# Optimization experiments

Hardware: AMD Instinct MI355X
Metric: run time of the kernel (lower is better)

## Reference

```python
import jax, jax.numpy as jnp
import numpy as np

B, N, D, H = 2, 4096, 512, 8
DH = D // H
FF = 4 * D
SCALE = D ** (-0.5)  # standard_scale=False -> dim**-0.5
EPS = 1e-5


def layernorm(x, w, b):
    mu = jnp.mean(x, axis=-1, keepdims=True)
    var = jnp.mean(jnp.square(x - mu), axis=-1, keepdims=True)
    return (x - mu) * jax.lax.rsqrt(var + EPS) * w + b


def setup_inputs() -> dict:
    key = jax.random.key(0)
    ks = jax.random.split(key, 12)
    s = lambda fin: 1.0 / np.sqrt(fin)
    return {
        "x": jax.random.normal(ks[0], (B, N, D), jnp.float32),
        "gamma": jax.random.uniform(ks[1], (B,), jnp.float32),
        "dist": jax.random.uniform(ks[2], (N, N), jnp.float32),
        "ln1_w": jnp.ones((D,), jnp.float32),
        "ln1_b": jnp.zeros((D,), jnp.float32),
        "qkv_w": jax.random.normal(ks[3], (D, 3 * D), jnp.float32) * s(D),
        "qkv_b": jnp.zeros((3 * D,), jnp.float32),
        "proj_w": jax.random.normal(ks[4], (D, D), jnp.float32) * s(D),
        "proj_b": jnp.zeros((D,), jnp.float32),
        "ln2_w": jnp.ones((D,), jnp.float32),
        "ln2_b": jnp.zeros((D,), jnp.float32),
        "fc1_w": jax.random.normal(ks[5], (D, FF), jnp.float32) * s(D),
        "fc1_b": jnp.zeros((FF,), jnp.float32),
        "fc2_w": jax.random.normal(ks[6], (FF, D), jnp.float32) * s(FF),
        "fc2_b": jnp.zeros((D,), jnp.float32),
    }


def reference(x, gamma, dist, ln1_w, ln1_b, qkv_w, qkv_b, proj_w, proj_b,
              ln2_w, ln2_b, fc1_w, fc1_b, fc2_w, fc2_b):
    # --- attention branch ---
    h = layernorm(x, ln1_w, ln1_b)                       # [B,N,D]
    qkv = h @ qkv_w + qkv_b                              # [B,N,3D]
    qkv = qkv.reshape(B, N, 3, H, DH).transpose(2, 0, 3, 1, 4)  # [3,B,H,N,DH]
    q, k, v = qkv[0], qkv[1], qkv[2]
    scores = jnp.einsum('bhnd,bhmd->bhnm', q, k) * SCALE
    scores = scores - gamma[:, None, None, None] * dist[None, None]
    w = jax.nn.softmax(scores, axis=-1)                  # [B,H,N,N]
    out = jnp.einsum('bhnm,bhmd->bhnd', w, v)            # [B,H,N,DH]
    out = out.transpose(0, 2, 1, 3).reshape(B, N, D)
    x = x + out @ proj_w + proj_b
    # --- MLP branch ---
    h = layernorm(x, ln2_w, ln2_b)
    h = jax.nn.gelu(h @ fc1_w + fc1_b, approximate=False)
    x = x + h @ fc2_w + fc2_b
    return x
```

## Files before the change

### kernel.cpp

```cpp
#include <hip/hip_runtime.h>
#include <math.h>

typedef __bf16 bf16x8 __attribute__((ext_vector_type(8)));
typedef __bf16 bf16x4 __attribute__((ext_vector_type(4)));
typedef float  f32x4  __attribute__((ext_vector_type(4)));
typedef unsigned int u32x4 __attribute__((ext_vector_type(4)));

#define B_   2
#define N_   4096
#define D_   512
#define H_   8
#define FF_  2048
#define BN_  (B_*N_)
static constexpr float SCALE_ = 0.04419417382415922f;
static constexpr float LOG2E_ = 1.44269504088896341f;
static constexpr float SCALE_L2E_ = SCALE_ * LOG2E_;

#define GLOAD_LDS16(g, l) __builtin_amdgcn_global_load_lds( \
    (const __attribute__((address_space(1))) void*)(g),     \
    (__attribute__((address_space(3))) void*)(l), 16, 0, 0)

__global__ void transpose_to_bf16(const float* __restrict__ in, __bf16* __restrict__ out,
                                  int R, int C) {
    __shared__ float tile[32][33];
    const int c0 = blockIdx.x * 32, r0 = blockIdx.y * 32;
    const int tx = threadIdx.x, ty = threadIdx.y;
#pragma unroll
    for (int i = 0; i < 4; ++i)
        tile[ty + 8*i][tx] = in[(size_t)(r0 + ty + 8*i) * C + c0 + tx];
    __syncthreads();
#pragma unroll
    for (int i = 0; i < 4; ++i)
        out[(size_t)(c0 + ty + 8*i) * R + r0 + tx] = (__bf16)tile[tx][ty + 8*i];
}

__global__ void cvt_bf16(const float* __restrict__ in, __bf16* __restrict__ out, int n4) {
    int i = blockIdx.x * blockDim.x + threadIdx.x;
    const int stride = gridDim.x * blockDim.x;
    for (; i < n4; i += stride) {
        float4 v = ((const float4*)in)[i];
        bf16x4 o;
        o[0] = (__bf16)(v.x * LOG2E_); o[1] = (__bf16)(v.y * LOG2E_);
        o[2] = (__bf16)(v.z * LOG2E_); o[3] = (__bf16)(v.w * LOG2E_);
        ((bf16x4*)out)[i] = o;
    }
}

__global__ __launch_bounds__(128)
void ln_kernel(const float* __restrict__ x, const float* __restrict__ w,
               const float* __restrict__ b, __bf16* __restrict__ out) {
    const int row = blockIdx.x, t = threadIdx.x;
    const float4 v = *(const float4*)&x[(size_t)row * 512 + t * 4];
    float s  = v.x + v.y + v.z + v.w;
    float sq = v.x*v.x + v.y*v.y + v.z*v.z + v.w*v.w;
#pragma unroll
    for (int mk = 1; mk < 64; mk <<= 1) { s += __shfl_xor(s, mk); sq += __shfl_xor(sq, mk); }
    __shared__ float ps[2][2];
    if ((t & 63) == 0) { ps[t >> 6][0] = s; ps[t >> 6][1] = sq; }
    __syncthreads();
    s = ps[0][0] + ps[1][0]; sq = ps[0][1] + ps[1][1];
    const float mu  = s * (1.0f / 512.0f);
    const float var = sq * (1.0f / 512.0f) - mu * mu;
    const float rs  = rsqrtf(var + 1e-5f);
    const float4 wv = *(const float4*)&w[t * 4];
    const float4 bv = *(const float4*)&b[t * 4];
    bf16x4 o;
    o[0] = (__bf16)((v.x - mu) * rs * wv.x + bv.x);
    o[1] = (__bf16)((v.y - mu) * rs * wv.y + bv.y);
    o[2] = (__bf16)((v.z - mu) * rs * wv.z + bv.z);
    o[3] = (__bf16)((v.w - mu) * rs * wv.w + bv.w);
    *(bf16x4*)&out[(size_t)row * 512 + t * 4] = o;
}

template<int EPI, int BNT, bool DBUF>
__global__ __launch_bounds__(256)
void gemm_bt(const __bf16* __restrict__ A, const __bf16* __restrict__ Bt,
             const float* __restrict__ bias, const float* __restrict__ resid,
             __bf16* __restrict__ outb, float* __restrict__ outf,
             int M, int N, int K) {
    constexpr int NI = BNT / 32;
    constexpr int NB = DBUF ? 2 : 1;
    __shared__ __align__(16) __bf16 As[NB][128 * 64];
    __shared__ __align__(16) __bf16 Bs[NB][BNT * 64];
    const int tid = threadIdx.x;
    const int w = tid >> 6, l = tid & 63;
    const int g = l >> 4, c = l & 15;
    const int m0 = blockIdx.y * 128, n0 = blockIdx.x * BNT;
    const int wm = (w >> 1) * 64, wn = (w & 1) * (BNT / 2);
    f32x4 acc[4][NI] = {};

    auto stage = [&](int kt, int buf) {
#pragma unroll
        for (int i = 0; i < 4; ++i) {
            const int cb = (i * 4 + w) * 64;
            const int chunk = cb + l;
            const int row = chunk >> 3, c8 = chunk & 7;
            GLOAD_LDS16(A + (size_t)(m0 + row) * K + kt + c8 * 8, As[buf] + cb * 8);
        }
#pragma unroll
        for (int i = 0; i < BNT / 32; ++i) {
            const int cb = (i * 4 + w) * 64;
            const int chunk = cb + l;
            const int row = chunk >> 3, c8 = chunk & 7;
            GLOAD_LDS16(Bt + (size_t)(n0 + row) * K + kt + c8 * 8, Bs[buf] + cb * 8);
        }
    };
    auto compute = [&](int buf) {
#pragma unroll
        for (int kk = 0; kk < 2; ++kk) {
            bf16x8 av[4], bv[NI];
#pragma unroll
            for (int mi = 0; mi < 4; ++mi)
                av[mi] = *(const bf16x8*)&As[buf][(wm + mi * 16 + c) * 64 + kk * 32 + g * 8];
#pragma unroll
            for (int ni = 0; ni < NI; ++ni)
                bv[ni] = *(const bf16x8*)&Bs[buf][(wn + ni * 16 + c) * 64 + kk * 32 + g * 8];
#pragma unroll
            for (int mi = 0; mi < 4; ++mi)
#pragma unroll
                for (int ni = 0; ni < NI; ++ni)
                    acc[mi][ni] = __builtin_amdgcn_mfma_f32_16x16x32_bf16(
                        av[mi], bv[ni], acc[mi][ni], 0, 0, 0);
        }
    };

    if constexpr (DBUF) {
        stage(0, 0);
        const int T = K / 64;
        for (int t = 0; t < T; ++t) {
            const int cur = t & 1;
            __syncthreads();
            if (t + 1 < T) stage((t + 1) * 64, cur ^ 1);
            compute(cur);
        }
    } else {
        for (int kt = 0; kt < K; kt += 64) {
            __syncthreads();
            stage(kt, 0);
            __syncthreads();
            compute(0);
        }
    }
#pragma unroll
    for (int mi = 0; mi < 4; ++mi)
#pragma unroll
        for (int ni = 0; ni < NI; ++ni)
#pragma unroll
            for (int r = 0; r < 4; ++r) {
                const int row = m0 + wm + mi * 16 + g * 4 + r;
                const int col = n0 + wn + ni * 16 + c;
                float v = acc[mi][ni][r] + bias[col];
                const size_t oidx = (size_t)row * N + col;
                if constexpr (EPI == 0) {
                    outb[oidx] = (__bf16)v;
                } else if constexpr (EPI == 1) {
                    outb[oidx] = (__bf16)(0.5f * v * (1.0f + erff(v * 0.70710678118654752f)));
                } else {
                    outf[oidx] = v + resid[oidx];
                }
            }
}

__global__ __launch_bounds__(512, 4)
void attn_kernel(const __bf16* __restrict__ qkv, const __bf16* __restrict__ distb,
                 const float* __restrict__ gamma, __bf16* __restrict__ outp) {
    __shared__ __align__(16) __bf16 Ks [64 * 64];
    __shared__ __align__(16) __bf16 Vts[64][72];
    __shared__ __align__(16) __bf16 DPs[2][128 * 64];
    const int tid = threadIdx.x;
    const int w = tid >> 6, l = tid & 63;
    const int g = l >> 4, c = l & 15;
    const int wq = w & 3, hn = w >> 2;
    const int qt = blockIdx.x, h = blockIdx.y;
    const int b = blockIdx.z;
    const float gb = gamma[b];
    const size_t tok0 = (size_t)b * N_;
    const int qrow = 16 * wq + c;
    const int wub = tid & 448;
    const int srow = tid >> 3;
    const int sd0  = (tid & 7) * 8;
    const int cswz = ((tid & 7) ^ (srow & 7)) * 8;
    const int swz  = (c & 7) << 3;

    bf16x8 qf[2][2];
#pragma unroll
    for (int t = 0; t < 2; ++t) {
        const size_t qbase = (tok0 + qt * 128 + 64 * t + qrow) * 1536 + h * 64;
#pragma unroll
        for (int kk = 0; kk < 2; ++kk) {
            const bf16x8 qv = *(const bf16x8*)&qkv[qbase + kk * 32 + g * 8];
#pragma unroll
            for (int j = 0; j < 8; ++j) qf[t][kk][j] = (__bf16)((float)qv[j] * SCALE_L2E_);
        }
    }
    bf16x8 ones;
#pragma unroll
    for (int j = 0; j < 8; ++j) ones[j] = (__bf16)1.0f;

    f32x4 acc[2][4] = {};
    f32x4 accl[2] = {};
    bf16x8 vreg;

    const size_t kvstep = (size_t)64 * 1536;
    const __bf16* gk = qkv + 512  + (tok0 + srow) * 1536 + h * 64 + cswz;
    const __bf16* gv = qkv + 1024 + (tok0 + srow) * 1536 + h * 64 + sd0;
    const __bf16* gd = distb + (size_t)(qt * 128 + srow) * N_ + cswz;

    auto issue_k = [&]() {
        GLOAD_LDS16(gk, Ks + wub * 8);
        gk += kvstep;
    };
    auto issue_d = [&](int buf) {
        GLOAD_LDS16(gd,                    DPs[buf] + wub * 8);
        GLOAD_LDS16(gd + (size_t)64 * N_,  DPs[buf] + (512 + wub) * 8);
        gd += 64;
    };
    auto issue_v = [&]() {
        vreg = *(const bf16x8*)gv;
        gv += kvstep;
    };
    auto write_vts = [&]() {
        const int kp = srow ^ sd0;
#pragma unroll
        for (int j = 0; j < 8; ++j) Vts[sd0 + j][kp] = vreg[j];
    };

    const int ktend = N_ / 64;
    issue_k();
    issue_v();
    issue_d(0);

    for (int kt = 0; kt < ktend; ++kt) {
        const int cur = kt & 1;
        __syncthreads();
        write_vts();
        if (kt + 1 < ktend) {
            issue_v();
            issue_d(cur ^ 1);
        }
        __builtin_amdgcn_sched_barrier(0);

        uint32_t W[2][2][2];
#pragma unroll
        for (int nii = 0; nii < 2; ++nii) {
            const int ni = 2 * hn + nii;
            f32x4 s0, s1;
            {
                const bf16x4 dd0 = *(const bf16x4*)
                    &DPs[cur][(qrow << 6) + ((16 * ni + 4 * g) ^ swz)];
                const bf16x4 dd1 = *(const bf16x4*)
                    &DPs[cur][((64 + qrow) << 6) + ((16 * ni + 4 * g) ^ swz)];
#pragma unroll
                for (int r = 0; r < 4; ++r) {
                    s0[r] = -gb * (float)dd0[r];
                    s1[r] = -gb * (float)dd1[r];
                }
            }
            __builtin_amdgcn_s_setprio(1);
#pragma unroll
            for (int kk = 0; kk < 2; ++kk) {
                const bf16x8 kf = *(const bf16x8*)
                    &Ks[((16 * ni + c) << 6) + ((kk * 32 + g * 8) ^ swz)];
                s0 = __builtin_amdgcn_mfma_f32_16x16x32_bf16(kf, qf[0][kk], s0, 0, 0, 0);
                s1 = __builtin_amdgcn_mfma_f32_16x16x32_bf16(kf, qf[1][kk], s1, 0, 0, 0);
            }
            __builtin_amdgcn_s_setprio(0);
#pragma unroll
            for (int t = 0; t < 2; ++t) {
                const f32x4 sv = (t == 0) ? s0 : s1;
                float pv0, pv1, pv2, pv3;
                pv0 = __builtin_amdgcn_exp2f(sv[0]);
                pv1 = __builtin_amdgcn_exp2f(sv[1]);
                pv2 = __builtin_amdgcn_exp2f(sv[2]);
                pv3 = __builtin_amdgcn_exp2f(sv[3]);
                asm("v_cvt_pk_bf16_f32 %0, %1, %2" : "=v"(W[t][nii][0]) : "v"(pv0), "v"(pv1));
                asm("v_cvt_pk_bf16_f32 %0, %1, %2" : "=v"(W[t][nii][1]) : "v"(pv2), "v"(pv3));
            }
        }
        bf16x8 pa[2];
#pragma unroll
        for (int t = 0; t < 2; ++t) {
#pragma unroll
            for (int p = 0; p < 2; ++p) {
                asm("v_permlane32_swap_b32 %0, %1"
                    : "+v"(W[t][0][p]), "+v"(W[t][1][p]));
                asm("v_permlane16_swap_b32 %0, %1"
                    : "+v"(W[t][0][p]), "+v"(W[t][1][p]));
            }
            const u32x4 words = {W[t][0][0], W[t][0][1], W[t][1][0], W[t][1][1]};
            pa[t] = __builtin_bit_cast(bf16x8, words);
        }
        __builtin_amdgcn_sched_barrier(0);
        asm volatile("s_waitcnt lgkmcnt(0)\n\ts_barrier" ::: "memory");
        __builtin_amdgcn_sched_barrier(0);
        if (kt + 1 < ktend) issue_k();

        __builtin_amdgcn_s_setprio(1);
        accl[0] = __builtin_amdgcn_mfma_f32_16x16x32_bf16(ones, pa[0], accl[0], 0, 0, 0);
        accl[1] = __builtin_amdgcn_mfma_f32_16x16x32_bf16(ones, pa[1], accl[1], 0, 0, 0);
#pragma unroll
        for (int di = 0; di < 4; ++di) {
            const int d = 16 * di + c;
            const int kp = (hn * 32 + g * 8) ^ ((d >> 3) << 3);
            const bf16x8 vb = *(const bf16x8*)&Vts[d][kp];
            acc[0][di] = __builtin_amdgcn_mfma_f32_16x16x32_bf16(vb, pa[0], acc[0][di], 0, 0, 0);
            acc[1][di] = __builtin_amdgcn_mfma_f32_16x16x32_bf16(vb, pa[1], acc[1][di], 0, 0, 0);
        }
        __builtin_amdgcn_s_setprio(0);
    }

    __syncthreads();
    float* sacc = (float*)&DPs[0][0];
    float* sl   = (float*)&Ks[0];
    const int slot = wq * 64 + l;
    if (hn == 0) {
#pragma unroll
        for (int t = 0; t < 2; ++t) {
            sl[slot * 2 + t] = accl[t][0];
#pragma unroll
            for (int di = 0; di < 4; ++di)
                *(f32x4*)&sacc[(slot * 8 + t * 4 + di) * 4] = acc[t][di];
        }
    }
    __syncthreads();
    if (hn == 1) {
#pragma unroll
        for (int t = 0; t < 2; ++t) {
            const float rl = 1.0f / (accl[t][0] + sl[slot * 2 + t]);
            const int q = qt * 128 + 64 * t + qrow;
#pragma unroll
            for (int di = 0; di < 4; ++di) {
                const f32x4 oa = acc[t][di] + *(const f32x4*)&sacc[(slot * 8 + t * 4 + di) * 4];
                bf16x4 o;
#pragma unroll
                for (int r = 0; r < 4; ++r) o[r] = (__bf16)(oa[r] * rl);
                *(bf16x4*)&outp[((size_t)(b * N_ + q)) * 512 + h * 64 + 16 * di + 4 * g] = o;
            }
        }
    }
}

extern "C" void kernel_launch(void* const* d_in, const int* in_sizes, int n_in,
                              void* d_out, int out_size, void* d_ws, size_t ws_size,
                              hipStream_t stream) {
    (void)in_sizes; (void)n_in; (void)out_size; (void)ws_size;
    const float* x      = (const float*)d_in[0];
    const float* gamma  = (const float*)d_in[1];
    const float* dist   = (const float*)d_in[2];
    const float* ln1_w  = (const float*)d_in[3];
    const float* ln1_b  = (const float*)d_in[4];
    const float* qkv_w  = (const float*)d_in[5];
    const float* qkv_b  = (const float*)d_in[6];
    const float* proj_w = (const float*)d_in[7];
    const float* proj_b = (const float*)d_in[8];
    const float* ln2_w  = (const float*)d_in[9];
    const float* ln2_b  = (const float*)d_in[10];
    const float* fc1_w  = (const float*)d_in[11];
    const float* fc1_b  = (const float*)d_in[12];
    const float* fc2_w  = (const float*)d_in[13];
    const float* fc2_b  = (const float*)d_in[14];
    float* out = (float*)d_out;

    char* ws = (char*)d_ws;
    size_t off = 0;
    auto alloc = [&](size_t bytes) {
        void* p = ws + off; off = (off + bytes + 255) & ~(size_t)255; return p;
    };
    __bf16* distbf  = (__bf16*)alloc((size_t)N_ * N_ * 2);
    __bf16* qkv_wt  = (__bf16*)alloc((size_t)1536 * 512 * 2);
    __bf16* proj_wt = (__bf16*)alloc((size_t)512 * 512 * 2);
    __bf16* fc1_wt  = (__bf16*)alloc((size_t)2048 * 512 * 2);
    __bf16* fc2_wt  = (__bf16*)alloc((size_t)512 * 2048 * 2);
    __bf16* hbuf    = (__bf16*)alloc((size_t)BN_ * 512 * 2);
    __bf16* qkvbuf  = (__bf16*)alloc((size_t)BN_ * 1536 * 2);
    __bf16* attnbuf = (__bf16*)alloc((size_t)BN_ * 512 * 2);
    float*  x1buf   = (float*) alloc((size_t)BN_ * 512 * 4);
    __bf16* h2buf   = (__bf16*)alloc((size_t)BN_ * 512 * 2);
    __bf16* ffbuf   = (__bf16*)alloc((size_t)BN_ * 2048 * 2);

    const dim3 tb(32, 8);
    transpose_to_bf16<<<dim3(1536/32,  512/32), tb, 0, stream>>>(qkv_w,  qkv_wt,  512, 1536);
    transpose_to_bf16<<<dim3( 512/32,  512/32), tb, 0, stream>>>(proj_w, proj_wt, 512,  512);
    transpose_to_bf16<<<dim3(2048/32,  512/32), tb, 0, stream>>>(fc1_w,  fc1_wt,  512, 2048);
    transpose_to_bf16<<<dim3( 512/32, 2048/32), tb, 0, stream>>>(fc2_w,  fc2_wt, 2048,  512);
    cvt_bf16<<<2048, 256, 0, stream>>>(dist, distbf, N_ * N_ / 4);

    ln_kernel<<<BN_, 128, 0, stream>>>(x, ln1_w, ln1_b, hbuf);
    gemm_bt<0,128,false><<<dim3(1536/128, BN_/128), 256, 0, stream>>>(
        hbuf, qkv_wt, qkv_b, nullptr, qkvbuf, nullptr, BN_, 1536, 512);
    attn_kernel<<<dim3(32, 8, 2), 512, 0, stream>>>(qkvbuf, distbf, gamma, attnbuf);
    gemm_bt<2,64,true><<<dim3(512/64, BN_/128), 256, 0, stream>>>(
        attnbuf, proj_wt, proj_b, x, nullptr, x1buf, BN_, 512, 512);
    ln_kernel<<<BN_, 128, 0, stream>>>(x1buf, ln2_w, ln2_b, h2buf);
    gemm_bt<1,128,false><<<dim3(2048/128, BN_/128), 256, 0, stream>>>(
        h2buf, fc1_wt, fc1_b, nullptr, ffbuf, nullptr, BN_, 2048, 512);
    gemm_bt<2,64,true><<<dim3(512/64, BN_/128), 256, 0, stream>>>(
        ffbuf, fc2_wt, fc2_b, x1buf, nullptr, out, BN_, 512, 2048);
}
```

Baseline: 284.5 us.

## Stage GEMM epilogue through LDS for vectorized stores; drop double buffering

Reworks the GEMM epilogue so each wave first writes its accumulator tile into LDS, reusing the A tile buffer. It then reads the tile back in row-contiguous chunks and issues 16-byte vector stores and residual loads, replacing scattered scalar per-element stores. It also adds a min-blocks-per-CU hint of 4 to launch_bounds and switches the two N=512 GEMMs from double-buffered to single-buffered staging to cut LDS use and raise occupancy. The trade-off is an extra LDS round trip plus a barrier in the epilogue, and loss of load/compute overlap in the proj and fc2 GEMMs.

```diff
diff --git a/kernel.cpp b/kernel.cpp
--- a/kernel.cpp
+++ b/kernel.cpp
@@ -73,7 +73,7 @@
 }
 
 template<int EPI, int BNT, bool DBUF>
-__global__ __launch_bounds__(256)
+__global__ __launch_bounds__(256, 4)
 void gemm_bt(const __bf16* __restrict__ A, const __bf16* __restrict__ Bt,
              const float* __restrict__ bias, const float* __restrict__ resid,
              __bf16* __restrict__ outb, float* __restrict__ outf,
@@ -141,24 +141,53 @@
             compute(0);
         }
     }
-#pragma unroll
-    for (int mi = 0; mi < 4; ++mi)
-#pragma unroll
-        for (int ni = 0; ni < NI; ++ni)
-#pragma unroll
-            for (int r = 0; r < 4; ++r) {
-                const int row = m0 + wm + mi * 16 + g * 4 + r;
-                const int col = n0 + wn + ni * 16 + c;
-                float v = acc[mi][ni][r] + bias[col];
-                const size_t oidx = (size_t)row * N + col;
-                if constexpr (EPI == 0) {
-                    outb[oidx] = (__bf16)v;
-                } else if constexpr (EPI == 1) {
-                    outb[oidx] = (__bf16)(0.5f * v * (1.0f + erff(v * 0.70710678118654752f)));
-                } else {
-                    outf[oidx] = v + resid[oidx];
+
+    __syncthreads();
+    if constexpr (EPI == 2) {
+        constexpr int LDW = NI * 16 + 4;
+        float* ep = (float*)&As[0][0] + w * (16 * LDW);
+#pragma unroll
+        for (int mi = 0; mi < 4; ++mi) {
+#pragma unroll
+            for (int ni = 0; ni < NI; ++ni)
+#pragma unroll
+                for (int r = 0; r < 4; ++r)
+                    ep[(g * 4 + r) * LDW + ni * 16 + c] =
+                        acc[mi][ni][r] + bias[n0 + wn + ni * 16 + c];
+#pragma unroll
+            for (int rnd = 0; rnd < NI; ++rnd) {
+                const int idx = rnd * 64 + l;
+                const int rr = idx >> 3, cc = idx & 7;
+                const f32x4 vv = *(const f32x4*)&ep[rr * LDW + cc * 4];
+                const size_t oidx = (size_t)(m0 + wm + mi * 16 + rr) * N + n0 + wn + cc * 4;
+                const f32x4 rv = *(const f32x4*)&resid[oidx];
+                *(f32x4*)&outf[oidx] = vv + rv;
+            }
+        }
+    } else {
+        constexpr int LDW = NI * 16 + 8;
+        __bf16* ep = &As[0][0] + w * (16 * LDW);
+#pragma unroll
+        for (int mi = 0; mi < 4; ++mi) {
+#pragma unroll
+            for (int ni = 0; ni < NI; ++ni)
+#pragma unroll
+                for (int r = 0; r < 4; ++r) {
+                    float v = acc[mi][ni][r] + bias[n0 + wn + ni * 16 + c];
+                    if constexpr (EPI == 1)
+                        v = 0.5f * v * (1.0f + erff(v * 0.70710678118654752f));
+                    ep[(g * 4 + r) * LDW + ni * 16 + c] = (__bf16)v;
                 }
-            }
+#pragma unroll
+            for (int rnd = 0; rnd < NI / 2; ++rnd) {
+                const int idx = rnd * 64 + l;
+                const int rr = idx >> 3, cc = idx & 7;
+                const bf16x8 vv = *(const bf16x8*)&ep[rr * LDW + cc * 8];
+                const size_t oidx = (size_t)(m0 + wm + mi * 16 + rr) * N + n0 + wn + cc * 8;
+                *(bf16x8*)&outb[oidx] = vv;
+            }
+        }
+    }
 }
 
 __global__ __launch_bounds__(512, 4)
@@ -389,11 +418,11 @@
     gemm_bt<0,128,false><<<dim3(1536/128, BN_/128), 256, 0, stream>>>(
         hbuf, qkv_wt, qkv_b, nullptr, qkvbuf, nullptr, BN_, 1536, 512);
     attn_kernel<<<dim3(32, 8, 2), 512, 0, stream>>>(qkvbuf, distbf, gamma, attnbuf);
-    gemm_bt<2,64,true><<<dim3(512/64, BN_/128), 256, 0, stream>>>(
+    gemm_bt<2,64,false><<<dim3(512/64, BN_/128), 256, 0, stream>>>(
         attnbuf, proj_wt, proj_b, x, nullptr, x1buf, BN_, 512, 512);
     ln_kernel<<<BN_, 128, 0, stream>>>(x1buf, ln2_w, ln2_b, h2buf);
     gemm_bt<1,128,false><<<dim3(2048/128, BN_/128), 256, 0, stream>>>(
         h2buf, fc1_wt, fc1_b, nullptr, ffbuf, nullptr, BN_, 2048, 512);
-    gemm_bt<2,64,true><<<dim3(512/64, BN_/128), 256, 0, stream>>>(
+    gemm_bt<2,64,false><<<dim3(512/64, BN_/128), 256, 0, stream>>>(
         ffbuf, fc2_wt, fc2_b, x1buf, nullptr, out, BN_, 512, 2048);
 }
```

Result: faster. 262.3 us (-7.8%).
